# Performance work log

Hardware: AMD Instinct MI355X
Metric: run time of the kernel (lower is better)

Reference implementation:

```python
import jax, jax.numpy as jnp
import numpy as np

N_NODES = 100000
N_EDGES = 1600000
N_FEAT = 128
HIDDEN = 128
N_GRAPHS = 1024


def setup_inputs() -> dict:
    key = jax.random.key(0)
    ks = jax.random.split(key, 9)
    x = jax.random.normal(ks[0], (N_NODES, N_FEAT), dtype=jnp.float32)
    edge_index = jax.random.randint(ks[1], (2, N_EDGES), 0, N_NODES, dtype=jnp.int64)
    batch = jnp.sort(jax.random.randint(ks[2], (N_NODES,), 0, N_GRAPHS, dtype=jnp.int64))
    W1 = jax.random.normal(ks[3], (N_FEAT, HIDDEN), dtype=jnp.float32) * (1.0 / np.sqrt(N_FEAT))
    b1 = jax.random.normal(ks[4], (HIDDEN,), dtype=jnp.float32) * 0.01
    W2 = jax.random.normal(ks[5], (HIDDEN, HIDDEN), dtype=jnp.float32) * (1.0 / np.sqrt(HIDDEN))
    b2 = jax.random.normal(ks[6], (HIDDEN,), dtype=jnp.float32) * 0.01
    Wl = jax.random.normal(ks[7], (HIDDEN, 2), dtype=jnp.float32) * (1.0 / np.sqrt(HIDDEN))
    bl = jax.random.normal(ks[8], (2,), dtype=jnp.float32) * 0.01
    return {"x": x, "edge_index": edge_index, "batch": batch,
            "W1": W1, "b1": b1, "W2": W2, "b2": b2, "Wl": Wl, "bl": bl}


def _gcn_norm(edge_index, num_nodes):
    # PyG GCNConv: add self-loops, then sym-normalize with in-degree (target col).
    loop = jnp.arange(num_nodes, dtype=edge_index.dtype)
    src = jnp.concatenate([edge_index[0], loop])  # [E+N]
    dst = jnp.concatenate([edge_index[1], loop])  # [E+N]
    deg = jax.ops.segment_sum(jnp.ones_like(dst, dtype=jnp.float32), dst,
                              num_segments=num_nodes)
    dinv = jnp.where(deg > 0, jax.lax.rsqrt(deg), 0.0)
    norm = dinv[src] * dinv[dst]  # [E+N]
    return src, dst, norm


def _gcn_conv(h, W, b, src, dst, norm, num_nodes):
    h = h @ W                                   # [N, out]
    msg = h[src] * norm[:, None]                # gather + scale, [E+N, out]
    agg = jax.ops.segment_sum(msg, dst, num_segments=num_nodes)  # scatter-add
    return agg + b


def reference(x, edge_index, batch, W1, b1, W2, b2, Wl, bl):
    n = x.shape[0]
    src, dst, norm = _gcn_norm(edge_index, n)
    h = jax.nn.relu(_gcn_conv(x, W1, b1, src, dst, norm, n))
    h = jax.nn.relu(_gcn_conv(h, W2, b2, src, dst, norm, n))
    # global_mean_pool over graph ids
    sums = jax.ops.segment_sum(h, batch, num_segments=N_GRAPHS)        # [G, H]
    counts = jax.ops.segment_sum(jnp.ones((n,), jnp.float32), batch,
                                 num_segments=N_GRAPHS)
    pooled = sums / jnp.maximum(counts, 1.0)[:, None]
    # F.dropout with training=False default in inference -> identity
    return pooled @ Wl + bl  # [G, 2]
```

## Files before the change

kernel.cpp:

```cpp
#include <hip/hip_runtime.h>
#include <hip/hip_bf16.h>

#define N_NODES 100000
#define N_EDGES 1600000
#define FEAT 128
#define N_GRAPHS 1024
#define NBUCK 391
#define CHUNK 4096
#define NTILES 1563
#define G1A 781
#define G1B 782

typedef short short8 __attribute__((ext_vector_type(8)));
typedef float float4v __attribute__((ext_vector_type(4)));

static __device__ inline unsigned short f2bf(float f) {
    __hip_bfloat16 b = __float2bfloat16(f);
    unsigned short r;
    __builtin_memcpy(&r, &b, 2);
    return r;
}
static __device__ inline float bf_lo(unsigned int v) { return __uint_as_float(v << 16); }
static __device__ inline float bf_hi(unsigned int v) { return __uint_as_float(v & 0xFFFF0000u); }
static __device__ inline float bf_s(unsigned short s) { return __uint_as_float(((unsigned)s) << 16); }

__global__ __launch_bounds__(256) void k_prep_hist(const float* __restrict__ W1,
                                                   const float* __restrict__ W2,
                                                   unsigned short* __restrict__ wp1,
                                                   unsigned short* __restrict__ wp2,
                                                   const int* __restrict__ dst,
                                                   int* __restrict__ bcount,
                                                   unsigned int* __restrict__ udummy,
                                                   float* __restrict__ dinv) {
    int bid = blockIdx.x;
    if (bid < 128) {
        const float* W = (bid < 64) ? W1 : W2;
        unsigned short* wp = (bid < 64) ? wp1 : wp2;
        int t = (bid & 63) * 256 + threadIdx.x;
        int k = t >> 7, n = t & 127;
        float w = W[k * 128 + n];
        unsigned ub = __float_as_uint(w);
        unsigned short hi = (unsigned short)(ub >> 16);
        float hif = __uint_as_float(ub & 0xFFFF0000u);
        unsigned short lo = f2bf(w - hif);
        int sidx = n * 128 + ((k & 7) | (8 * (((k >> 3) ^ n) & 15)));
        wp[sidx] = hi;
        wp[16384 + sidx] = lo;
        if (bid == 0) {
            if (threadIdx.x < 64) udummy[threadIdx.x] = 0;
            if (threadIdx.x == 64) dinv[N_NODES] = 0.f;
        }
    } else {
        __shared__ int h[NBUCK];
        for (int i = threadIdx.x; i < NBUCK; i += 256) h[i] = 0;
        __syncthreads();
        int hb = bid - 128;
        for (int e = hb * 256 + threadIdx.x; e < N_EDGES; e += 256 * 256)
            atomicAdd(&h[dst[e] >> 8], 1);
        __syncthreads();
        for (int i = threadIdx.x; i < NBUCK; i += 256) {
            int c = h[i];
            if (c) atomicAdd(&bcount[i], c);
        }
    }
}

__global__ __launch_bounds__(512) void k_scan391(const int* __restrict__ in,
                                                 int* __restrict__ base,
                                                 int* __restrict__ cur,
                                                 int* __restrict__ tail) {
    int t = threadIdx.x;
    int v = (t < NBUCK) ? in[t] : 0;
    int lane = t & 63, wid = t >> 6;
    int s = v;
#pragma unroll
    for (int d = 1; d < 64; d <<= 1) { int n = __shfl_up(s, d); if (lane >= d) s += n; }
    __shared__ int ws[8];
    if (lane == 63) ws[wid] = s;
    __syncthreads();
    if (t < 8) {
        int x = ws[t];
#pragma unroll
        for (int d = 1; d < 8; d <<= 1) { int n = __shfl_up(x, d); if ((int)t >= d) x += n; }
        ws[t] = x;
    }
    __syncthreads();
    int excl = s - v + (wid ? ws[wid - 1] : 0);
    if (t < NBUCK) {
        base[t] = excl;
        cur[t] = excl;
    }
    if (t == 0) tail[0] = N_EDGES;
}

__device__ __forceinline__ void gemm_f32_body(int tile, const float* __restrict__ inp,
                                              const unsigned short* __restrict__ wp,
                                              unsigned short* __restrict__ u) {
    __shared__ unsigned short sW[32768];
    {
        float4* d4 = (float4*)sW;
        const float4* s4 = (const float4*)wp;
#pragma unroll
        for (int i = 0; i < 16; ++i) d4[threadIdx.x + 256 * i] = s4[threadIdx.x + 256 * i];
    }
    __syncthreads();
    const int t = threadIdx.x;
    const int wv = t >> 6, L = t & 63;
    const int m = L & 15, q = L >> 4;
    const int r0 = tile * 64 + wv * 16;
    int arow = r0 + m;
    if (arow >= N_NODES) arow = N_NODES - 1;
    const float4* ap = (const float4*)(inp + (size_t)arow * 128);
    float4v acc[8];
#pragma unroll
    for (int c = 0; c < 8; ++c) acc[c] = (float4v){0.f, 0.f, 0.f, 0.f};
#pragma unroll
    for (int k0 = 0; k0 < 128; k0 += 32) {
        float4 f0 = ap[(k0 >> 2) + 2 * q];
        float4 f1 = ap[(k0 >> 2) + 2 * q + 1];
        float fa[8] = {f0.x, f0.y, f0.z, f0.w, f1.x, f1.y, f1.z, f1.w};
        short8 ah, al;
#pragma unroll
        for (int j = 0; j < 8; ++j) {
            unsigned ub = __float_as_uint(fa[j]);
            ah[j] = (short)(ub >> 16);
            float hif = __uint_as_float(ub & 0xFFFF0000u);
            al[j] = (short)f2bf(fa[j] - hif);
        }
        const int b = (k0 >> 3) + q;
#pragma unroll
        for (int c = 0; c < 8; ++c) {
            int ng = c * 16 + m;
            int elem = ng * 128 + 8 * ((b ^ ng) & 15);
            short8 bh = *(const short8*)&sW[elem];
            short8 bl = *(const short8*)&sW[16384 + elem];
            acc[c] = __builtin_amdgcn_mfma_f32_16x16x32_bf16(ah, bh, acc[c], 0, 0, 0);
            acc[c] = __builtin_amdgcn_mfma_f32_16x16x32_bf16(al, bh, acc[c], 0, 0, 0);
            acc[c] = __builtin_amdgcn_mfma_f32_16x16x32_bf16(ah, bl, acc[c], 0, 0, 0);
        }
    }
#pragma unroll
    for (int r = 0; r < 4; ++r) {
        int row = r0 + 4 * q + r;
        if (row < N_NODES) {
            unsigned short* up = u + (size_t)row * 128 + m;
#pragma unroll
            for (int c = 0; c < 8; ++c) up[c * 16] = f2bf(acc[c][r]);
        }
    }
}

__global__ __launch_bounds__(256) void k_bucket_g1(const int* __restrict__ src,
                                                   const int* __restrict__ dst,
                                                   int* __restrict__ bcur,
                                                   unsigned int* __restrict__ pairs,
                                                   const float* __restrict__ x,
                                                   const unsigned short* __restrict__ wp1,
                                                   unsigned short* __restrict__ u) {
    if (blockIdx.x >= NBUCK) {
        gemm_f32_body(blockIdx.x - NBUCK, x, wp1, u);
        return;
    }
    __shared__ int cnt[NBUCK];
    __shared__ int basebuf[NBUCK];
    int t = threadIdx.x;
    int e0 = blockIdx.x * CHUNK;
    for (int i = t; i < NBUCK; i += 256) cnt[i] = 0;
    __syncthreads();
    unsigned pk[16]; int bk[16];
#pragma unroll
    for (int j = 0; j < 16; ++j) {
        int e = e0 + j * 256 + t;
        if (e < N_EDGES) {
            int s = src[e], d = dst[e];
            bk[j] = d >> 8;
            pk[j] = ((unsigned)s << 8) | (unsigned)(d & 255);
            atomicAdd(&cnt[bk[j]], 1);
        } else bk[j] = -1;
    }
    __syncthreads();
    for (int i = t; i < NBUCK; i += 256) {
        int c = cnt[i];
        basebuf[i] = c ? atomicAdd(&bcur[i], c) : 0;
        cnt[i] = 0;
    }
    __syncthreads();
#pragma unroll
    for (int j = 0; j < 16; ++j) {
        if (bk[j] >= 0) {
            int p = basebuf[bk[j]] + atomicAdd(&cnt[bk[j]], 1);
            pairs[p] = pk[j];
        }
    }
}

__global__ __launch_bounds__(256) void k_bfill_g1(const unsigned int* __restrict__ pairs,
                                                  const int* __restrict__ bbase,
                                                  const int* __restrict__ bcount,
                                                  float* __restrict__ dinv,
                                                  int* __restrict__ offs,
                                                  int* __restrict__ csr,
                                                  const float* __restrict__ x,
                                                  const unsigned short* __restrict__ wp1,
                                                  unsigned short* __restrict__ u) {
    if (blockIdx.x >= NBUCK) {
        gemm_f32_body(blockIdx.x - NBUCK + G1A, x, wp1, u);
        return;
    }
    __shared__ int degl[256];
    __shared__ int lcur[256];
    __shared__ int ws[4];
    int b = blockIdx.x, t = threadIdx.x;
    degl[t] = 0;
    __syncthreads();
    int s0 = bbase[b], n = bcount[b];
    for (int i = t; i < n; i += 256) atomicAdd(&degl[pairs[s0 + i] & 255u], 1);
    __syncthreads();
    int node = b * 256 + t;
    int dv = degl[t];
    if (node < N_NODES) dinv[node] = rsqrtf((float)(dv + 1));
    int lane = t & 63, wid = t >> 6;
    int s = dv;
#pragma unroll
    for (int d = 1; d < 64; d <<= 1) { int nn = __shfl_up(s, d); if (lane >= d) s += nn; }
    if (lane == 63) ws[wid] = s;
    __syncthreads();
    if (t < 4) {
        int xx = ws[t];
#pragma unroll
        for (int d = 1; d < 4; d <<= 1) { int nn = __shfl_up(xx, d); if ((int)t >= d) xx += nn; }
        ws[t] = xx;
    }
    __syncthreads();
    int excl = s - dv + (wid ? ws[wid - 1] : 0) + bbase[b];
    if (node < N_NODES) offs[node] = excl;
    lcur[t] = excl;
    __syncthreads();
    for (int i = t; i < n; i += 256) {
        unsigned pr = pairs[s0 + i];
        int p = atomicAdd(&lcur[pr & 255u], 1);
        csr[p] = (int)(pr >> 8);
    }
}

__global__ __launch_bounds__(256) void k_gemm_mfma_bf(const unsigned short* __restrict__ hh,
                                                      const unsigned short* __restrict__ hl,
                                                      const unsigned short* __restrict__ wp,
                                                      unsigned short* __restrict__ u) {
    __shared__ unsigned short sW[32768];
    {
        float4* d4 = (float4*)sW;
        const float4* s4 = (const float4*)wp;
#pragma unroll
        for (int i = 0; i < 16; ++i) d4[threadIdx.x + 256 * i] = s4[threadIdx.x + 256 * i];
    }
    __syncthreads();
    const int t = threadIdx.x;
    const int wv = t >> 6, L = t & 63;
    const int m = L & 15, q = L >> 4;
    const int r0 = blockIdx.x * 64 + wv * 16;
    int arow = r0 + m;
    if (arow >= N_NODES) arow = N_NODES - 1;
    const unsigned short* hhp = hh + (size_t)arow * 128 + 8 * q;
    const unsigned short* hlp = hl + (size_t)arow * 128 + 8 * q;
    float4v acc[8];
#pragma unroll
    for (int c = 0; c < 8; ++c) acc[c] = (float4v){0.f, 0.f, 0.f, 0.f};
#pragma unroll
    for (int k0 = 0; k0 < 128; k0 += 32) {
        short8 ah = *(const short8*)(hhp + k0);
        short8 al = *(const short8*)(hlp + k0);
        const int b = (k0 >> 3) + q;
#pragma unroll
        for (int c = 0; c < 8; ++c) {
            int ng = c * 16 + m;
            int elem = ng * 128 + 8 * ((b ^ ng) & 15);
            short8 bh = *(const short8*)&sW[elem];
            short8 bl = *(const short8*)&sW[16384 + elem];
            acc[c] = __builtin_amdgcn_mfma_f32_16x16x32_bf16(ah, bh, acc[c], 0, 0, 0);
            acc[c] = __builtin_amdgcn_mfma_f32_16x16x32_bf16(al, bh, acc[c], 0, 0, 0);
            acc[c] = __builtin_amdgcn_mfma_f32_16x16x32_bf16(ah, bl, acc[c], 0, 0, 0);
        }
    }
#pragma unroll
    for (int r = 0; r < 4; ++r) {
        int row = r0 + 4 * q + r;
        if (row < N_NODES) {
            unsigned short* up = u + (size_t)row * 128 + m;
#pragma unroll
            for (int c = 0; c < 8; ++c) up[c * 16] = f2bf(acc[c][r]);
        }
    }
}

__global__ __launch_bounds__(256) void k_agg(const unsigned int* __restrict__ u,
                                             const int* __restrict__ offs,
                                             const int* __restrict__ csr,
                                             const float* __restrict__ dinv,
                                             const float* __restrict__ bias,
                                             unsigned int* __restrict__ hhp,
                                             unsigned int* __restrict__ hlp) {
    int wid = threadIdx.x >> 6;
    int lane = threadIdx.x & 63;
    int node = __builtin_amdgcn_readfirstlane(blockIdx.x * 4 + wid);
    if (node >= N_NODES) return;
    int p = __builtin_amdgcn_readfirstlane(offs[node]);
    int e = __builtin_amdgcn_readfirstlane(offs[node + 1]);
    float dsf = dinv[node];
    unsigned int self = u[(size_t)node * 64 + lane];
    float ax0 = dsf * bf_lo(self), ay0 = dsf * bf_hi(self);
    float ax1 = 0.f, ay1 = 0.f, ax2 = 0.f, ay2 = 0.f, ax3 = 0.f, ay3 = 0.f;
    float ax4 = 0.f, ay4 = 0.f, ax5 = 0.f, ay5 = 0.f, ax6 = 0.f, ay6 = 0.f;
    float ax7 = 0.f, ay7 = 0.f;
    for (; p < e; p += 8) {
        int c0 = csr[p + 0], c1 = csr[p + 1], c2 = csr[p + 2], c3 = csr[p + 3];
        int c4 = csr[p + 4], c5 = csr[p + 5], c6 = csr[p + 6], c7 = csr[p + 7];
        int i0 = c0;
        int i1 = (p + 1 < e) ? c1 : N_NODES;
        int i2 = (p + 2 < e) ? c2 : N_NODES;
        int i3 = (p + 3 < e) ? c3 : N_NODES;
        int i4 = (p + 4 < e) ? c4 : N_NODES;
        int i5 = (p + 5 < e) ? c5 : N_NODES;
        int i6 = (p + 6 < e) ? c6 : N_NODES;
        int i7 = (p + 7 < e) ? c7 : N_NODES;
        float d0 = dinv[i0], d1 = dinv[i1], d2 = dinv[i2], d3 = dinv[i3];
        float d4 = dinv[i4], d5 = dinv[i5], d6 = dinv[i6], d7 = dinv[i7];
        unsigned v0 = (u + (size_t)i0 * 64)[lane];
        unsigned v1 = (u + (size_t)i1 * 64)[lane];
        unsigned v2 = (u + (size_t)i2 * 64)[lane];
        unsigned v3 = (u + (size_t)i3 * 64)[lane];
        unsigned v4 = (u + (size_t)i4 * 64)[lane];
        unsigned v5 = (u + (size_t)i5 * 64)[lane];
        unsigned v6 = (u + (size_t)i6 * 64)[lane];
        unsigned v7 = (u + (size_t)i7 * 64)[lane];
        ax0 = fmaf(d0, bf_lo(v0), ax0); ay0 = fmaf(d0, bf_hi(v0), ay0);
        ax1 = fmaf(d1, bf_lo(v1), ax1); ay1 = fmaf(d1, bf_hi(v1), ay1);
        ax2 = fmaf(d2, bf_lo(v2), ax2); ay2 = fmaf(d2, bf_hi(v2), ay2);
        ax3 = fmaf(d3, bf_lo(v3), ax3); ay3 = fmaf(d3, bf_hi(v3), ay3);
        ax4 = fmaf(d4, bf_lo(v4), ax4); ay4 = fmaf(d4, bf_hi(v4), ay4);
        ax5 = fmaf(d5, bf_lo(v5), ax5); ay5 = fmaf(d5, bf_hi(v5), ay5);
        ax6 = fmaf(d6, bf_lo(v6), ax6); ay6 = fmaf(d6, bf_hi(v6), ay6);
        ax7 = fmaf(d7, bf_lo(v7), ax7); ay7 = fmaf(d7, bf_hi(v7), ay7);
    }
    float2 b = ((const float2*)bias)[lane];
    float sx = ((ax0 + ax1) + (ax2 + ax3)) + ((ax4 + ax5) + (ax6 + ax7));
    float sy = ((ay0 + ay1) + (ay2 + ay3)) + ((ay4 + ay5) + (ay6 + ay7));
    float r0 = fmaxf(dsf * sx + b.x, 0.f);
    float r1 = fmaxf(dsf * sy + b.y, 0.f);
    if (hlp) {
        unsigned u0 = __float_as_uint(r0), u1 = __float_as_uint(r1);
        unsigned short h0 = (unsigned short)(u0 >> 16), h1 = (unsigned short)(u1 >> 16);
        float rf0 = __uint_as_float(u0 & 0xFFFF0000u), rf1 = __uint_as_float(u1 & 0xFFFF0000u);
        unsigned short l0 = f2bf(r0 - rf0), l1 = f2bf(r1 - rf1);
        hhp[(size_t)node * 64 + lane] = (unsigned)h0 | ((unsigned)h1 << 16);
        hlp[(size_t)node * 64 + lane] = (unsigned)l0 | ((unsigned)l1 << 16);
    } else {
        hhp[(size_t)node * 64 + lane] = (unsigned)f2bf(r0) | ((unsigned)f2bf(r1) << 16);
    }
}

__global__ __launch_bounds__(128) void k_pool(const unsigned short* __restrict__ hh,
                                              const int* __restrict__ batch,
                                              const float* __restrict__ Wl,
                                              const float* __restrict__ bl,
                                              float* __restrict__ out) {
    int g = blockIdx.x;
    int c = threadIdx.x;
    __shared__ int sb[2];
    if (c < 2) {
        int tgt = g + c;
        int lo = 0, hi = N_NODES;
        while (lo < hi) { int m = (lo + hi) >> 1; if (batch[m] < tgt) lo = m + 1; else hi = m; }
        sb[c] = lo;
    }
    __syncthreads();
    int s0 = sb[0], s1 = sb[1];
    float sum = 0.f;
    for (int i = s0; i < s1; ++i) sum += bf_s(hh[(size_t)i * 128 + c]);
    float cnt = (float)(s1 - s0);
    float pooled = sum / fmaxf(cnt, 1.0f);
    __shared__ float red[128];
    float w0 = Wl[c * 2 + 0], w1 = Wl[c * 2 + 1];
    red[c] = pooled * w0;
    __syncthreads();
    for (int st = 64; st > 0; st >>= 1) { if (c < st) red[c] += red[c + st]; __syncthreads(); }
    if (c == 0) out[g * 2 + 0] = red[0] + bl[0];
    __syncthreads();
    red[c] = pooled * w1;
    __syncthreads();
    for (int st = 64; st > 0; st >>= 1) { if (c < st) red[c] += red[c + st]; __syncthreads(); }
    if (c == 0) out[g * 2 + 1] = red[0] + bl[1];
}

extern "C" void kernel_launch(void* const* d_in, const int* in_sizes, int n_in,
                              void* d_out, int out_size, void* d_ws, size_t ws_size,
                              hipStream_t stream) {
    const float* x  = (const float*)d_in[0];
    const int* ei   = (const int*)d_in[1];
    const int* batch = (const int*)d_in[2];
    const float* W1 = (const float*)d_in[3];
    const float* b1 = (const float*)d_in[4];
    const float* W2 = (const float*)d_in[5];
    const float* b2 = (const float*)d_in[6];
    const float* Wl = (const float*)d_in[7];
    const float* bl = (const float*)d_in[8];
    float* out = (float*)d_out;
    const int* src = ei;
    const int* dst = ei + N_EDGES;

    char* ws = (char*)d_ws;
    size_t o = 0;
    auto alloc = [&](size_t bytes) -> void* {
        o = (o + 255) & ~(size_t)255;
        void* p = ws + o;
        o += bytes;
        return p;
    };
    int* bcount = (int*)alloc((size_t)NBUCK * 4);
    int* bbase  = (int*)alloc((size_t)NBUCK * 4);
    int* bcur   = (int*)alloc((size_t)NBUCK * 4);
    float* dinv = (float*)alloc((size_t)(N_NODES + 1) * 4);
    int* offs   = (int*)alloc((size_t)(N_NODES + 1) * 4);
    unsigned short* wp1 = (unsigned short*)alloc(65536);
    unsigned short* wp2 = (unsigned short*)alloc(65536);
    unsigned int* pairs = (unsigned int*)alloc((size_t)N_EDGES * 4);
    int* csr    = (int*)alloc((size_t)(N_EDGES + 8) * 4);
    unsigned short* u = (unsigned short*)alloc((size_t)(N_NODES + 1) * 128 * 2);
    unsigned short* hh = (unsigned short*)alloc((size_t)N_NODES * 128 * 2);
    unsigned short* hl = (unsigned short*)alloc((size_t)N_NODES * 128 * 2);

    hipMemsetAsync(bcount, 0, (size_t)NBUCK * 4, stream);
    k_prep_hist<<<384, 256, 0, stream>>>(W1, W2, wp1, wp2, dst, bcount,
                                         (unsigned int*)(u + (size_t)N_NODES * 128), dinv);
    k_scan391<<<1, 512, 0, stream>>>(bcount, bbase, bcur, &offs[N_NODES]);
    k_bucket_g1<<<NBUCK + G1A, 256, 0, stream>>>(src, dst, bcur, pairs, x, wp1, u);
    k_bfill_g1<<<NBUCK + G1B, 256, 0, stream>>>(pairs, bbase, bcount, dinv, offs, csr, x, wp1, u);

    k_agg<<<(N_NODES + 3) / 4, 256, 0, stream>>>((const unsigned int*)u, offs, csr, dinv, b1,
                                                 (unsigned int*)hh, (unsigned int*)hl);
    k_gemm_mfma_bf<<<NTILES, 256, 0, stream>>>(hh, hl, wp2, u);
    k_agg<<<(N_NODES + 3) / 4, 256, 0, stream>>>((const unsigned int*)u, offs, csr, dinv, b2,
                                                 (unsigned int*)hh, nullptr);

    k_pool<<<N_GRAPHS, 128, 0, stream>>>(hh, batch, Wl, bl, out);
}
```

Before: 354.4 us.

## Fuse mean-pool and final linear into second aggregation via per-node atomics

The second aggregation kernel now projects each node's hidden vector onto the two output logits with a wave shuffle reduction and atomically accumulates them into per-graph output slots, instead of storing the full hidden matrix. A small finalize kernel divides by graph node counts and adds the bias, replacing the separate pooling kernel. This removes a large intermediate write and re-read but adds global atomics and makes summation order nondeterministic.

After: 431.9 us. 1.22x slower.

```diff
diff --git a/kernel.cpp b/kernel.cpp
--- a/kernel.cpp
+++ b/kernel.cpp
@@ -299,7 +299,10 @@
                                              const float* __restrict__ dinv,
                                              const float* __restrict__ bias,
                                              unsigned int* __restrict__ hhp,
-                                             unsigned int* __restrict__ hlp) {
+                                             unsigned int* __restrict__ hlp,
+                                             const float* __restrict__ Wl,
+                                             float* __restrict__ outp,
+                                             const int* __restrict__ batch) {
     int wid = threadIdx.x >> 6;
     int lane = threadIdx.x & 63;
     int node = __builtin_amdgcn_readfirstlane(blockIdx.x * 4 + wid);
@@ -355,41 +358,36 @@
         hhp[(size_t)node * 64 + lane] = (unsigned)h0 | ((unsigned)h1 << 16);
         hlp[(size_t)node * 64 + lane] = (unsigned)l0 | ((unsigned)l1 << 16);
     } else {
-        hhp[(size_t)node * 64 + lane] = (unsigned)f2bf(r0) | ((unsigned)f2bf(r1) << 16);
-    }
-}
-
-__global__ __launch_bounds__(128) void k_pool(const unsigned short* __restrict__ hh,
-                                              const int* __restrict__ batch,
-                                              const float* __restrict__ Wl,
-                                              const float* __restrict__ bl,
-                                              float* __restrict__ out) {
-    int g = blockIdx.x;
-    int c = threadIdx.x;
-    __shared__ int sb[2];
-    if (c < 2) {
-        int tgt = g + c;
-        int lo = 0, hi = N_NODES;
-        while (lo < hi) { int m = (lo + hi) >> 1; if (batch[m] < tgt) lo = m + 1; else hi = m; }
-        sb[c] = lo;
-    }
-    __syncthreads();
-    int s0 = sb[0], s1 = sb[1];
-    float sum = 0.f;
-    for (int i = s0; i < s1; ++i) sum += bf_s(hh[(size_t)i * 128 + c]);
-    float cnt = (float)(s1 - s0);
-    float pooled = sum / fmaxf(cnt, 1.0f);
-    __shared__ float red[128];
-    float w0 = Wl[c * 2 + 0], w1 = Wl[c * 2 + 1];
-    red[c] = pooled * w0;
-    __syncthreads();
-    for (int st = 64; st > 0; st >>= 1) { if (c < st) red[c] += red[c + st]; __syncthreads(); }
-    if (c == 0) out[g * 2 + 0] = red[0] + bl[0];
-    __syncthreads();
-    red[c] = pooled * w1;
-    __syncthreads();
-    for (int st = 64; st > 0; st >>= 1) { if (c < st) red[c] += red[c + st]; __syncthreads(); }
-    if (c == 0) out[g * 2 + 1] = red[0] + bl[1];
+        float2 wl0 = ((const float2*)Wl)[2 * lane];
+        float2 wl1 = ((const float2*)Wl)[2 * lane + 1];
+        float p0 = r0 * wl0.x + r1 * wl1.x;
+        float p1 = r0 * wl0.y + r1 * wl1.y;
+#pragma unroll
+        for (int d = 32; d > 0; d >>= 1) {
+            p0 += __shfl_xor(p0, d);
+            p1 += __shfl_xor(p1, d);
+        }
+        if (lane == 0) {
+            int g = batch[node];
+            atomicAdd(&outp[2 * g + 0], p0);
+            atomicAdd(&outp[2 * g + 1], p1);
+        }
+    }
+}
+
+__global__ __launch_bounds__(256) void k_fin(const int* __restrict__ batch,
+                                             const float* __restrict__ bl,
+                                             float* __restrict__ out) {
+    int g = blockIdx.x * 256 + threadIdx.x;
+    if (g >= N_GRAPHS) return;
+    int lo = 0, hi = N_NODES;
+    while (lo < hi) { int m = (lo + hi) >> 1; if (batch[m] < g) lo = m + 1; else hi = m; }
+    int s0 = lo;
+    hi = N_NODES;
+    while (lo < hi) { int m = (lo + hi) >> 1; if (batch[m] < g + 1) lo = m + 1; else hi = m; }
+    float inv = 1.f / fmaxf((float)(lo - s0), 1.f);
+    out[2 * g + 0] = out[2 * g + 0] * inv + bl[0];
+    out[2 * g + 1] = out[2 * g + 1] * inv + bl[1];
 }
 
 extern "C" void kernel_launch(void* const* d_in, const int* in_sizes, int n_in,
@@ -430,6 +428,7 @@
     unsigned short* hl = (unsigned short*)alloc((size_t)N_NODES * 128 * 2);
 
     hipMemsetAsync(bcount, 0, (size_t)NBUCK * 4, stream);
+    hipMemsetAsync(out, 0, (size_t)N_GRAPHS * 2 * 4, stream);
     k_prep_hist<<<384, 256, 0, stream>>>(W1, W2, wp1, wp2, dst, bcount,
                                          (unsigned int*)(u + (size_t)N_NODES * 128), dinv);
     k_scan391<<<1, 512, 0, stream>>>(bcount, bbase, bcur, &offs[N_NODES]);
@@ -437,10 +436,11 @@
     k_bfill_g1<<<NBUCK + G1B, 256, 0, stream>>>(pairs, bbase, bcount, dinv, offs, csr, x, wp1, u);
 
     k_agg<<<(N_NODES + 3) / 4, 256, 0, stream>>>((const unsigned int*)u, offs, csr, dinv, b1,
-                                                 (unsigned int*)hh, (unsigned int*)hl);
+                                                 (unsigned int*)hh, (unsigned int*)hl,
+                                                 nullptr, nullptr, nullptr);
     k_gemm_mfma_bf<<<NTILES, 256, 0, stream>>>(hh, hl, wp2, u);
     k_agg<<<(N_NODES + 3) / 4, 256, 0, stream>>>((const unsigned int*)u, offs, csr, dinv, b2,
-                                                 (unsigned int*)hh, nullptr);
-
-    k_pool<<<N_GRAPHS, 128, 0, stream>>>(hh, batch, Wl, bl, out);
-}
+                                                 nullptr, nullptr, Wl, out, batch);
+
+    k_fin<<<(N_GRAPHS + 255) / 256, 256, 0, stream>>>(batch, bl, out);
+}
```
